# Kernel optimization log

Hardware: AMD Instinct MI355X
Metric: run time of the kernel (lower is better)

Reference implementation:

```python
import math
import jax, jax.numpy as jnp
import numpy as np

D_IN = 768      # input_hidden_dim
H = 512         # IDLU_hidden_dim
E = 64          # num_entity
B = 32          # batch_size (mentions)
P = 197         # num_patch (incl. CLS)
RHO = 4.0
EPS = 1e-5


def setup_inputs() -> dict:
    key = jax.random.key(0)
    ks = jax.random.split(key, 16)
    s = 1.0 / math.sqrt(D_IN)
    return {
        "entity_cls": jax.random.normal(ks[0], (E, D_IN), jnp.float32),
        "entity_tokens": jax.random.normal(ks[1], (E, P, D_IN), jnp.float32),
        "mention_image_cls": jax.random.normal(ks[2], (B, D_IN), jnp.float32),
        "mention_image_tokens": jax.random.normal(ks[3], (B, P, D_IN), jnp.float32),
        "mention_patch_mask": jax.random.uniform(ks[4], (B, P), jnp.float32),
        "Wq": jax.random.normal(ks[5], (D_IN, H), jnp.float32) * s,
        "bq": jnp.zeros((H,), jnp.float32),
        "Wk": jax.random.normal(ks[6], (D_IN, H), jnp.float32) * s,
        "bk": jnp.zeros((H,), jnp.float32),
        "Wv": jax.random.normal(ks[7], (D_IN, H), jnp.float32) * s,
        "bv": jnp.zeros((H,), jnp.float32),
        "Wcls": jax.random.normal(ks[8], (D_IN, H), jnp.float32) * s,
        "bcls": jnp.zeros((H,), jnp.float32),
        "ln_g": jnp.ones((H,), jnp.float32),
        "ln_b": jnp.zeros((H,), jnp.float32),
    }


def _layer_norm(x, g, b):
    mu = jnp.mean(x, axis=-1, keepdims=True)
    var = jnp.mean(jnp.square(x - mu), axis=-1, keepdims=True)
    return (x - mu) * jax.lax.rsqrt(var + EPS) * g + b


def reference(entity_cls, entity_tokens, mention_image_cls, mention_image_tokens,
              mention_patch_mask, Wq, bq, Wk, bk, Wv, bv, Wcls, bcls, ln_g, ln_b):
    entity_cls_fc = entity_cls @ Wcls + bcls                      # [E, H]
    q = entity_tokens @ Wq + bq                                   # [E, P, H]
    k = mention_image_tokens @ Wk + bk                            # [B, P, H]
    v = mention_image_tokens @ Wv + bv                            # [B, P, H]
    # broadcast entity x mention attention: [E, B, P, P]
    scores = jnp.einsum('eph,bqh->ebpq', q, k) / math.sqrt(H)
    # additive mask only on the first query row (CLS)
    scores = scores.at[:, :, 0, :].add(RHO * mention_patch_mask[None, :, :])
    probs = jax.nn.softmax(scores, axis=-1)                       # [E, B, P, P]
    context = jnp.einsum('ebpq,bqh->ebph', probs, v)              # [E, B, P, H]
    context = jnp.mean(context, axis=-2)                          # [E, B, H]
    context = _layer_norm(context, ln_g, ln_b)
    g2l = jnp.sum(entity_cls_fc[:, None, :] * context, axis=-1).T # [B, E]
    g2g = mention_image_cls @ entity_cls.T                        # [B, E]
    return (g2l + g2g) / 2
```

## Files before the change

### kernel.cpp

```cpp
#include <hip/hip_runtime.h>
#include <stdint.h>

#define EN 64
#define BN 32
#define PN 197
#define DIN 768
#define HH 512
#define RHO_ 4.0f

typedef __attribute__((ext_vector_type(8))) short bf16x8;
typedef __attribute__((ext_vector_type(4))) float f32x4;

__device__ __forceinline__ ushort f2bf(float f){
  unsigned u = __float_as_uint(f);
  u += 0x7FFFu + ((u >> 16) & 1u);
  return (ushort)(u >> 16);
}
__device__ __forceinline__ float bf2f(ushort h){ return __uint_as_float(((unsigned)h) << 16); }

__global__ __launch_bounds__(256) void prep_kernel(
    const float* __restrict__ etok, const float* __restrict__ mtok,
    const float* __restrict__ ecls,
    const float* __restrict__ Wq, const float* __restrict__ Wk,
    const float* __restrict__ Wv, const float* __restrict__ Wc,
    const float* __restrict__ bq,
    ushort* __restrict__ a_ent, ushort* __restrict__ a_men, ushort* __restrict__ a_cls,
    ushort* __restrict__ Wt, float* __restrict__ bq_s)
{
  const float s = 0.04419417382415922f;
  int g = blockIdx.x*256 + threadIdx.x;
  int st = gridDim.x*256;
  for (int i=g; i<(EN*PN*DIN)/4; i+=st){
    float4 v = ((const float4*)etok)[i];
    ushort4 o; o.x=f2bf(v.x); o.y=f2bf(v.y); o.z=f2bf(v.z); o.w=f2bf(v.w);
    ((ushort4*)a_ent)[i] = o;
  }
  for (int i=g; i<(BN*PN*DIN)/4; i+=st){
    float4 v = ((const float4*)mtok)[i];
    ushort4 o; o.x=f2bf(v.x); o.y=f2bf(v.y); o.z=f2bf(v.z); o.w=f2bf(v.w);
    ((ushort4*)a_men)[i] = o;
  }
  for (int i=g; i<(EN*DIN)/4; i+=st){
    float4 v = ((const float4*)ecls)[i];
    ushort4 o; o.x=f2bf(v.x); o.y=f2bf(v.y); o.z=f2bf(v.z); o.w=f2bf(v.w);
    ((ushort4*)a_cls)[i] = o;
  }
  for (int i=g; i<4*HH*DIN; i+=st){
    int mat = i / (HH*DIN);
    int j = i - mat*(HH*DIN);
    int n = j / DIN;
    int kk = j - n*DIN;
    const float* src = (mat==0)?Wq:(mat==1)?Wk:(mat==2)?Wv:Wc;
    float v = src[kk*HH + n];
    if (mat==0) v *= s;
    Wt[i] = f2bf(v);
  }
  for (int i=g; i<HH; i+=st) bq_s[i] = bq[i]*s;
}

__global__ __launch_bounds__(256) void gemm_proj(
    const ushort* __restrict__ a_ent, const ushort* __restrict__ a_men, const ushort* __restrict__ a_cls,
    const ushort* __restrict__ Wt,
    const float* __restrict__ bq_s, const float* __restrict__ bk,
    const float* __restrict__ bv, const float* __restrict__ bc,
    ushort* __restrict__ qo, ushort* __restrict__ ko, ushort* __restrict__ vo,
    float* __restrict__ co)
{
  int x = blockIdx.x;
  int op, mt;
  if (x < 99)        { op = 0; mt = x; }
  else if (x < 149)  { op = 1; mt = x - 99; }
  else if (x < 199)  { op = 2; mt = x - 149; }
  else               { op = 3; mt = 0; }
  int M = (op==0)? EN*PN : (op==3)? EN : BN*PN;
  int m0 = mt*128;
  const ushort* A  = (op==0)? a_ent : (op==3)? a_cls : a_men;
  const ushort* Bw = Wt + (size_t)op*HH*DIN;
  const float* bias = (op==0)? bq_s : (op==1)? bk : (op==2)? bv : bc;
  int n0 = blockIdx.y*128;
  int Mm1 = M-1;

  __shared__ ushort As[128*40];
  __shared__ ushort Bs[128*40];
  int tid = threadIdx.x;
  int lane = tid & 63, wid = tid >> 6;
  int l15 = lane & 15, lg = lane >> 4;
  int wm = wid >> 1, wn = wid & 1;

  f32x4 acc[16];
  #pragma unroll
  for (int i=0;i<16;++i){ f32x4 z = {0.f,0.f,0.f,0.f}; acc[i] = z; }

  bf16x8 sA[2], sB[2];
  #pragma unroll
  for (int i=0;i<2;++i){
    int u = tid + i*256; int row = u>>2; int ko8 = (u&3)*8;
    int rA = m0+row; rA = rA>Mm1 ? Mm1 : rA;
    sA[i] = *(const bf16x8*)(A  + (size_t)rA*DIN + ko8);
    sB[i] = *(const bf16x8*)(Bw + (size_t)(n0+row)*DIN + ko8);
  }
  for (int kt=0; kt<DIN/32; ++kt){
    #pragma unroll
    for (int i=0;i<2;++i){
      int u = tid + i*256; int row = u>>2; int ko8 = (u&3)*8;
      *(bf16x8*)(&As[row*40 + ko8]) = sA[i];
      *(bf16x8*)(&Bs[row*40 + ko8]) = sB[i];
    }
    __syncthreads();
    if (kt < DIN/32 - 1){
      int k0 = (kt+1)*32;
      #pragma unroll
      for (int i=0;i<2;++i){
        int u = tid + i*256; int row = u>>2; int ko8 = (u&3)*8;
        int rA = m0+row; rA = rA>Mm1 ? Mm1 : rA;
        sA[i] = *(const bf16x8*)(A  + (size_t)rA*DIN + k0 + ko8);
        sB[i] = *(const bf16x8*)(Bw + (size_t)(n0+row)*DIN + k0 + ko8);
      }
    }
    bf16x8 af[4], bfg[4];
    #pragma unroll
    for (int t=0;t<4;++t){
      af[t]  = *(const bf16x8*)(&As[(wm*64 + t*16 + l15)*40 + lg*8]);
      bfg[t] = *(const bf16x8*)(&Bs[(wn*64 + t*16 + l15)*40 + lg*8]);
    }
    #pragma unroll
    for (int am=0; am<4; ++am)
      #pragma unroll
      for (int bn=0; bn<4; ++bn)
        acc[am*4+bn] = __builtin_amdgcn_mfma_f32_16x16x32_bf16(af[am], bfg[bn], acc[am*4+bn], 0, 0, 0);
    __syncthreads();
  }

  #pragma unroll
  for (int bn=0; bn<4; ++bn){
    int col = n0 + wn*64 + bn*16 + l15;
    float bval = bias[col];
    #pragma unroll
    for (int am=0; am<4; ++am){
      #pragma unroll
      for (int r=0;r<4;++r){
        int row = m0 + wm*64 + am*16 + lg*4 + r;
        if (row < M){
          float v = acc[am*4+bn][r] + bval;
          if (op==3)      co[(size_t)row*HH + col] = v;
          else if (op==0) qo[(size_t)row*HH + col] = f2bf(v);
          else if (op==1) ko[(size_t)row*HH + col] = f2bf(v);
          else            vo[(size_t)row*HH + col] = f2bf(v);
        }
      }
    }
  }
}

__global__ __launch_bounds__(512, 2) void attn_kernel(
    const ushort* __restrict__ qw, const ushort* __restrict__ kw, const ushort* __restrict__ vw,
    const float* __restrict__ cls_fc, const float* __restrict__ maskp,
    const float* __restrict__ mcls, const float* __restrict__ ecls,
    const float* __restrict__ lng, const float* __restrict__ lnb,
    float* __restrict__ outp)
{
  int bid = blockIdx.x;
  int b = bid >> 5;
  int e0 = (bid & 31) * 2;

  __shared__ ushort klds[2][112*256];
  __shared__ float w_lds[2][208];
  __shared__ float red[32];

  int tid = threadIdx.x;
  int lane = tid & 63, wid = tid >> 6;
  int l15 = lane & 15, lg = (lane >> 4) & 3;

  for (int i=tid; i<416; i+=512) ((float*)w_lds)[i] = 0.f;

  const ushort* kb  = kw + (size_t)b*PN*HH;
  const ushort* qb0 = qw + (size_t)e0*PN*HH;
  const ushort* qb1 = qw + (size_t)(e0+1)*PN*HH;

  bf16x8 stg[7];
  bf16x8 afr[2][8];

  for (int rnd=0; rnd<2; ++rnd){
    int tt = rnd*8 + wid;
    bool active = tt < 13;
    int rt = active ? tt : 12;
    int arow = rt*16 + l15;
    int arowg = arow > 196 ? 196 : arow;

    f32x4 acc[2][13];
    #pragma unroll
    for (int e2=0;e2<2;++e2)
      #pragma unroll
      for (int i=0;i<13;++i){ f32x4 z={0.f,0.f,0.f,0.f}; acc[e2][i]=z; }

    #pragma unroll
    for (int i=0;i<7;++i){
      int u = tid + i*512; int col = u>>5, o32 = u&31;
      int cg = col > 196 ? 196 : col;
      stg[i] = *(const bf16x8*)(kb + (size_t)cg*HH + o32*8);
    }

    for (int c=0; c<4; ++c){
      int kh = c>>1, ch = c&1;
      __syncthreads();
      #pragma unroll
      for (int i=0;i<7;++i){
        int u = tid + i*512; int col = u>>5, o32 = u&31;
        *(bf16x8*)(&klds[ch][col*256 + ((o32 ^ (col&7))*8)]) = stg[i];
      }
      __syncthreads();
      if (c < 3){
        int nkh = (c+1)>>1, ncb = ((c+1)&1)*112;
        #pragma unroll
        for (int i=0;i<7;++i){
          int u = tid + i*512; int col = u>>5, o32 = u&31;
          int cg = ncb + col; cg = cg > 196 ? 196 : cg;
          stg[i] = *(const bf16x8*)(kb + (size_t)cg*HH + nkh*256 + o32*8);
        }
      }
      if (ch == 0 && active){
        #pragma unroll
        for (int lc=0; lc<8; ++lc){
          afr[0][lc] = *(const bf16x8*)(qb0 + (size_t)arowg*HH + kh*256 + lc*32 + lg*8);
          afr[1][lc] = *(const bf16x8*)(qb1 + (size_t)arowg*HH + kh*256 + lc*32 + lg*8);
        }
      }
      if (active){
        if (ch == 0){
          #pragma unroll
          for (int ct=0; ct<7; ++ct){
            int lcol = ct*16 + l15, sw = lcol & 7;
            #pragma unroll
            for (int lc=0; lc<8; ++lc){
              bf16x8 bfr = *(const bf16x8*)(&klds[0][lcol*256 + (((lc*4+lg) ^ sw)*8)]);
              acc[0][ct] = __builtin_amdgcn_mfma_f32_16x16x32_bf16(afr[0][lc], bfr, acc[0][ct], 0,0,0);
              acc[1][ct] = __builtin_amdgcn_mfma_f32_16x16x32_bf16(afr[1][lc], bfr, acc[1][ct], 0,0,0);
            }
          }
        } else {
          #pragma unroll
          for (int ct=0; ct<6; ++ct){
            int lcol = ct*16 + l15, sw = lcol & 7;
            #pragma unroll
            for (int lc=0; lc<8; ++lc){
              bf16x8 bfr = *(const bf16x8*)(&klds[1][lcol*256 + (((lc*4+lg) ^ sw)*8)]);
              acc[0][7+ct] = __builtin_amdgcn_mfma_f32_16x16x32_bf16(afr[0][lc], bfr, acc[0][7+ct], 0,0,0);
              acc[1][7+ct] = __builtin_amdgcn_mfma_f32_16x16x32_bf16(afr[1][lc], bfr, acc[1][7+ct], 0,0,0);
            }
          }
        }
      }
    }

    if (active){
      #pragma unroll
      for (int e2=0; e2<2; ++e2){
        if (l15 >= 5){
          f32x4 ninf = {-1e30f,-1e30f,-1e30f,-1e30f};
          acc[e2][12] = ninf;
        }
        if (rt==0 && lg==0){
          #pragma unroll
          for (int ct=0; ct<13; ++ct){
            int col = ct*16 + l15;
            if (col < 197) acc[e2][ct][0] += RHO_ * maskp[b*PN + col];
          }
        }
        float mrow[4], inv[4];
        #pragma unroll
        for (int r=0;r<4;++r){
          float m = acc[e2][0][r];
          #pragma unroll
          for (int ct=1; ct<13; ++ct) m = fmaxf(m, acc[e2][ct][r]);
          m = fmaxf(m, __shfl_xor(m,1));
          m = fmaxf(m, __shfl_xor(m,2));
          m = fmaxf(m, __shfl_xor(m,4));
          m = fmaxf(m, __shfl_xor(m,8));
          mrow[r] = m;
        }
        #pragma unroll
        for (int r=0;r<4;++r){
          float s = 0.f;
          #pragma unroll
          for (int ct=0; ct<13; ++ct){
            float ev = __expf(acc[e2][ct][r] - mrow[r]);
            acc[e2][ct][r] = ev;
            s += ev;
          }
          s += __shfl_xor(s,1); s += __shfl_xor(s,2);
          s += __shfl_xor(s,4); s += __shfl_xor(s,8);
          int prow = rt*16 + lg*4 + r;
          inv[r] = (prow < PN) ? 1.0f/s : 0.f;
        }
        #pragma unroll
        for (int ct=0; ct<13; ++ct){
          float cs = acc[e2][ct][0]*inv[0] + acc[e2][ct][1]*inv[1]
                   + acc[e2][ct][2]*inv[2] + acc[e2][ct][3]*inv[3];
          cs += __shfl_xor(cs,16);
          cs += __shfl_xor(cs,32);
          if (lg==0) atomicAdd(&w_lds[e2][ct*16 + l15], cs);
        }
      }
    }
  }
  __syncthreads();

  const ushort* vb = vw + (size_t)b*PN*HH;
  float cA=0.f, cB=0.f;
  #pragma unroll 4
  for (int q=0; q<PN; ++q){
    float vq = bf2f(vb[(size_t)q*HH + tid]);
    cA += w_lds[0][q]*vq;
    cB += w_lds[1][q]*vq;
  }
  const float invP = 1.0f/197.0f;
  cA*=invP; cB*=invP;

  float sx = cA, sxx = cA*cA, sy = cB, syy = cB*cB;
  #pragma unroll
  for (int off=32; off; off>>=1){
    sx += __shfl_down(sx, off); sxx += __shfl_down(sxx, off);
    sy += __shfl_down(sy, off); syy += __shfl_down(syy, off);
  }
  if (lane==0){ red[wid*4+0]=sx; red[wid*4+1]=sxx; red[wid*4+2]=sy; red[wid*4+3]=syy; }
  __syncthreads();
  float s1A=0.f, s2A=0.f, s1B=0.f, s2B=0.f;
  #pragma unroll
  for (int w=0; w<8; ++w){
    s1A += red[w*4+0]; s2A += red[w*4+1];
    s1B += red[w*4+2]; s2B += red[w*4+3];
  }
  float muA = s1A*(1.f/512.f), muB = s1B*(1.f/512.f);
  float varA = s2A*(1.f/512.f) - muA*muA;
  float varB = s2B*(1.f/512.f) - muB*muB;
  float rsA = rsqrtf(varA + 1e-5f), rsB = rsqrtf(varB + 1e-5f);

  int h = tid;
  float g0=lng[h], bb0=lnb[h];
  float dA = ((cA-muA)*rsA*g0 + bb0) * cls_fc[(size_t)e0*HH + h];
  float dB = ((cB-muB)*rsB*g0 + bb0) * cls_fc[(size_t)(e0+1)*HH + h];

  dA += mcls[b*DIN + tid]*ecls[(size_t)e0*DIN + tid];
  dB += mcls[b*DIN + tid]*ecls[(size_t)(e0+1)*DIN + tid];
  if (tid < 256){
    int j = tid + 512;
    dA += mcls[b*DIN + j]*ecls[(size_t)e0*DIN + j];
    dB += mcls[b*DIN + j]*ecls[(size_t)(e0+1)*DIN + j];
  }

  __syncthreads();
  #pragma unroll
  for (int off=32; off; off>>=1){ dA += __shfl_down(dA, off); dB += __shfl_down(dB, off); }
  if (lane==0){ red[wid*2+0]=dA; red[wid*2+1]=dB; }
  __syncthreads();
  if (tid==0){
    float oA=0.f, oB=0.f;
    #pragma unroll
    for (int w=0; w<8; ++w){ oA += red[w*2+0]; oB += red[w*2+1]; }
    outp[b*EN + e0]   = 0.5f*oA;
    outp[b*EN + e0+1] = 0.5f*oB;
  }
}

extern "C" void kernel_launch(void* const* d_in, const int* in_sizes, int n_in,
                              void* d_out, int out_size, void* d_ws, size_t ws_size,
                              hipStream_t stream)
{
  (void)in_sizes; (void)n_in; (void)out_size; (void)ws_size;
  const float* ecls = (const float*)d_in[0];
  const float* etok = (const float*)d_in[1];
  const float* mcls = (const float*)d_in[2];
  const float* mtok = (const float*)d_in[3];
  const float* maskp= (const float*)d_in[4];
  const float* Wq   = (const float*)d_in[5];
  const float* bq   = (const float*)d_in[6];
  const float* Wk   = (const float*)d_in[7];
  const float* bk   = (const float*)d_in[8];
  const float* Wv   = (const float*)d_in[9];
  const float* bv   = (const float*)d_in[10];
  const float* Wc   = (const float*)d_in[11];
  const float* bc   = (const float*)d_in[12];
  const float* lng  = (const float*)d_in[13];
  const float* lnb  = (const float*)d_in[14];

  char* ws = (char*)d_ws;
  size_t off = 0;
  auto take = [&](size_t bytes){ char* p = ws + off; off += (bytes + 255) & ~(size_t)255; return p; };
  ushort* a_ent = (ushort*)take((size_t)EN*PN*DIN*2);
  ushort* a_men = (ushort*)take((size_t)BN*PN*DIN*2);
  ushort* a_cls = (ushort*)take((size_t)EN*DIN*2);
  ushort* Wt    = (ushort*)take((size_t)4*HH*DIN*2);
  float*  bq_s  = (float*)take((size_t)HH*4);
  ushort* qo    = (ushort*)take((size_t)EN*PN*HH*2);
  ushort* ko    = (ushort*)take((size_t)BN*PN*HH*2);
  ushort* vo    = (ushort*)take((size_t)BN*PN*HH*2);
  float*  co    = (float*)take((size_t)EN*HH*4);

  prep_kernel<<<2048, 256, 0, stream>>>(etok, mtok, ecls, Wq, Wk, Wv, Wc, bq,
                                        a_ent, a_men, a_cls, Wt, bq_s);
  gemm_proj<<<dim3(200,4,1), 256, 0, stream>>>(a_ent, a_men, a_cls, Wt,
                                               bq_s, bk, bv, bc, qo, ko, vo, co);
  attn_kernel<<<1024, 512, 0, stream>>>(qo, ko, vo, co, maskp, mcls, ecls,
                                        lng, lnb, (float*)d_out);
}
```

Measured before the change: 557.3 us.

## Split weight transpose into LDS-tiled kernel and relax attention launch bounds

The strided, uncoalesced weight transpose-and-convert loop moves out of the prep kernel into a dedicated kernel. That kernel stages 64x64 tiles in shared memory so global reads and writes are both coalesced. The prep grid is halved, and the attention kernel drops its minimum-blocks-per-CU hint from its launch bounds, which may change register allocation and occupancy. The aim is to remove the cost of strided global reads of the four weight matrices, at the price of one extra kernel launch.

```diff
diff --git a/kernel.cpp b/kernel.cpp
--- a/kernel.cpp
+++ b/kernel.cpp
@@ -20,16 +20,13 @@
 
 __global__ __launch_bounds__(256) void prep_kernel(
     const float* __restrict__ etok, const float* __restrict__ mtok,
-    const float* __restrict__ ecls,
-    const float* __restrict__ Wq, const float* __restrict__ Wk,
-    const float* __restrict__ Wv, const float* __restrict__ Wc,
-    const float* __restrict__ bq,
+    const float* __restrict__ ecls, const float* __restrict__ bq,
     ushort* __restrict__ a_ent, ushort* __restrict__ a_men, ushort* __restrict__ a_cls,
-    ushort* __restrict__ Wt, float* __restrict__ bq_s)
+    float* __restrict__ bq_s)
 {
-  const float s = 0.04419417382415922f;
   int g = blockIdx.x*256 + threadIdx.x;
   int st = gridDim.x*256;
+  const float s = 0.04419417382415922f;
   for (int i=g; i<(EN*PN*DIN)/4; i+=st){
     float4 v = ((const float4*)etok)[i];
     ushort4 o; o.x=f2bf(v.x); o.y=f2bf(v.y); o.z=f2bf(v.z); o.w=f2bf(v.w);
@@ -45,17 +42,34 @@
     ushort4 o; o.x=f2bf(v.x); o.y=f2bf(v.y); o.z=f2bf(v.z); o.w=f2bf(v.w);
     ((ushort4*)a_cls)[i] = o;
   }
-  for (int i=g; i<4*HH*DIN; i+=st){
-    int mat = i / (HH*DIN);
-    int j = i - mat*(HH*DIN);
-    int n = j / DIN;
-    int kk = j - n*DIN;
-    const float* src = (mat==0)?Wq:(mat==1)?Wk:(mat==2)?Wv:Wc;
-    float v = src[kk*HH + n];
-    if (mat==0) v *= s;
-    Wt[i] = f2bf(v);
-  }
   for (int i=g; i<HH; i+=st) bq_s[i] = bq[i]*s;
+}
+
+__global__ __launch_bounds__(256) void w_transpose(
+    const float* __restrict__ Wq, const float* __restrict__ Wk,
+    const float* __restrict__ Wv, const float* __restrict__ Wc,
+    ushort* __restrict__ Wt)
+{
+  __shared__ float tl[64][65];
+  int mat = blockIdx.z;
+  const float* src = (mat==0)?Wq:(mat==1)?Wk:(mat==2)?Wv:Wc;
+  float sc = (mat==0)? 0.04419417382415922f : 1.0f;
+  int k0 = blockIdx.x*64;
+  int n0 = blockIdx.y*64;
+  int tid = threadIdx.x;
+  int c = tid & 63, r0 = tid >> 6;
+  #pragma unroll
+  for (int i=0;i<16;++i){
+    int r = r0 + i*4;
+    tl[r][c] = src[(size_t)(k0+r)*HH + n0+c];
+  }
+  __syncthreads();
+  ushort* dst = Wt + (size_t)mat*HH*DIN;
+  #pragma unroll
+  for (int i=0;i<16;++i){
+    int r = r0 + i*4;
+    dst[(size_t)(n0+r)*DIN + k0+c] = f2bf(tl[c][r]*sc);
+  }
 }
 
 __global__ __launch_bounds__(256) void gemm_proj(
@@ -152,7 +166,7 @@
   }
 }
 
-__global__ __launch_bounds__(512, 2) void attn_kernel(
+__global__ __launch_bounds__(512) void attn_kernel(
     const ushort* __restrict__ qw, const ushort* __restrict__ kw, const ushort* __restrict__ vw,
     const float* __restrict__ cls_fc, const float* __restrict__ maskp,
     const float* __restrict__ mcls, const float* __restrict__ ecls,
@@ -396,8 +410,8 @@
   ushort* vo    = (ushort*)take((size_t)BN*PN*HH*2);
   float*  co    = (float*)take((size_t)EN*HH*4);
 
-  prep_kernel<<<2048, 256, 0, stream>>>(etok, mtok, ecls, Wq, Wk, Wv, Wc, bq,
-                                        a_ent, a_men, a_cls, Wt, bq_s);
+  prep_kernel<<<1024, 256, 0, stream>>>(etok, mtok, ecls, bq, a_ent, a_men, a_cls, bq_s);
+  w_transpose<<<dim3(12,8,4), 256, 0, stream>>>(Wq, Wk, Wv, Wc, Wt);
   gemm_proj<<<dim3(200,4,1), 256, 0, stream>>>(a_ent, a_men, a_cls, Wt,
                                                bq_s, bk, bv, bc, qo, ko, vo, co);
   attn_kernel<<<1024, 512, 0, stream>>>(qo, ko, vo, co, maskp, mcls, ecls,
```

Result: no change. 554.9 us (-0.4%).
